# Performance work log

Measured on AMD Instinct MI355X. Metric: run time of the kernel, lower is better.

The kernel has to match this reference:

```python
import jax, jax.numpy as jnp
import numpy as np

N_HEAD = 16
HIDDEN = 1024

def setup_inputs() -> dict:
    key = jax.random.key(0)
    ks = jax.random.split(key, 4)
    B, T, D = 2, 2048, HIDDEN
    x = jax.random.normal(ks[0], (B, T, D), dtype=jnp.float32)
    attention_mask = jnp.zeros((B, 1, 1, T), dtype=jnp.float32)  # additive mask
    w_attn = jax.random.normal(ks[1], (D, 3 * D), dtype=jnp.float32) * (1.0 / np.sqrt(D))
    b_attn = jnp.zeros((3 * D,), dtype=jnp.float32)
    w_proj = jax.random.normal(ks[2], (D, D), dtype=jnp.float32) * (1.0 / np.sqrt(D))
    b_proj = jnp.zeros((D,), dtype=jnp.float32)
    return {"x": x, "attention_mask": attention_mask,
            "w_attn": w_attn, "b_attn": b_attn,
            "w_proj": w_proj, "b_proj": b_proj}

def reference(x, attention_mask, w_attn, b_attn, w_proj, b_proj):
    B, T, D = x.shape
    H = N_HEAD
    hd = D // H
    qkv = x @ w_attn + b_attn                      # [B,T,3D]
    q, k, v = jnp.split(qkv, 3, axis=-1)
    q = q.reshape(B, T, H, hd)
    k = k.reshape(B, T, H, hd)
    v = v.reshape(B, T, H, hd)
    qk = jnp.einsum('BFNH,BTNH->BNFT', q, k) / jnp.sqrt(jnp.asarray(hd, qk_dtype := q.dtype))
    # NOTE: source adds the mask twice (once unconditionally, once inside the None-check)
    attn_weights = qk + attention_mask + attention_mask
    attn_probs = jax.nn.softmax(attn_weights, axis=-1)  # dropout(0.01) is identity at inference
    attn_out = jnp.einsum('BNFT,BTNH->BFNH', attn_probs, v)
    attn_out = attn_out.reshape(B, T, D)
    return attn_out @ w_proj + b_proj
```

## Files before the change

kernel.cpp:

```cpp
#include <hip/hip_runtime.h>
#include <hip/hip_bf16.h>

#define T_SEQ 2048
#define D_MODEL 1024
#define N_HEADS 16

typedef _Float16 half8 __attribute__((ext_vector_type(8)));
typedef _Float16 half4 __attribute__((ext_vector_type(4)));
typedef _Float16 half2v __attribute__((ext_vector_type(2)));
typedef float floatx4 __attribute__((ext_vector_type(4)));
typedef unsigned short ushort4v __attribute__((ext_vector_type(4)));
typedef unsigned short ushort8v __attribute__((ext_vector_type(8)));

#define LOG2E 1.44269504088896f

__device__ __forceinline__ unsigned short f32_to_bf16(float f) {
  unsigned u = __builtin_bit_cast(unsigned, f);
  u = u + 0x7FFFu + ((u >> 16) & 1u);
  return (unsigned short)(u >> 16);
}
__device__ __forceinline__ float bf16_to_f32(unsigned short h) {
  unsigned u = ((unsigned)h) << 16;
  return __builtin_bit_cast(float, u);
}
__device__ __forceinline__ half2v pk_f16(float a, float b) {
  return __builtin_bit_cast(half2v, __builtin_amdgcn_cvt_pkrtz(a, b));
}

__device__ __forceinline__ void load16_lds(const _Float16* g, _Float16* lds_base, int lane) {
#if __has_builtin(__builtin_amdgcn_global_load_lds)
  __builtin_amdgcn_global_load_lds(
      (const __attribute__((address_space(1))) void*)g,
      (__attribute__((address_space(3))) void*)lds_base, 16, 0, 0);
#else
  *(half8*)(lds_base + lane * 8) = *(const half8*)g;
#endif
}

__global__ void k_detect(const unsigned short* __restrict__ x, int* __restrict__ flag) {
  __shared__ int cnt;
  if (threadIdx.x == 0) cnt = 0;
  __syncthreads();
  unsigned short v = x[(size_t)threadIdx.x * 2];
  int e = (v >> 7) & 0xFF;
  int ok = (v == 0) || (e >= 100 && e <= 150);
  atomicAdd(&cnt, ok);
  __syncthreads();
  if (threadIdx.x == 0) *flag = (cnt >= 192) ? 1 : 0;
}

__global__ void k_cvt_h8(const void* __restrict__ in, _Float16* __restrict__ out,
                         int n8, const int* __restrict__ flag) {
  int f = *flag;
  int i = blockIdx.x * 256 + threadIdx.x;
  if (i >= n8) return;
  half8 o;
  if (f) {
    ushort8v u = ((const ushort8v*)in)[i];
#pragma unroll
    for (int e = 0; e < 8; ++e) o[e] = (_Float16)bf16_to_f32(u[e]);
  } else {
    floatx4 a = ((const floatx4*)in)[2 * i];
    floatx4 b = ((const floatx4*)in)[2 * i + 1];
#pragma unroll
    for (int e = 0; e < 4; ++e) { o[e] = (_Float16)a[e]; o[e + 4] = (_Float16)b[e]; }
  }
  ((half8*)out)[i] = o;
}

__global__ void k_cvt3(const void* __restrict__ ba, const void* __restrict__ bp,
                       const void* __restrict__ mk, float* __restrict__ baF,
                       float* __restrict__ bpF, float* __restrict__ mask2,
                       const int* __restrict__ flag) {
  int f = *flag;
  int i = blockIdx.x * 256 + threadIdx.x;
  auto cv = [&](const void* p, int j) {
    return f ? bf16_to_f32(((const unsigned short*)p)[j]) : ((const float*)p)[j];
  };
  if (i < 3072) baF[i] = cv(ba, i);
  else if (i < 4096) bpF[i - 3072] = cv(bp, i - 3072);
  else mask2[i - 4096] = cv(mk, i - 4096) * (2.0f * LOG2E);
}

__global__ __launch_bounds__(256) void k_transpose2(
    const void* __restrict__ inA, _Float16* __restrict__ outA,
    const void* __restrict__ inB, _Float16* __restrict__ outB,
    const int* __restrict__ flag) {
  __shared__ float tile[32][33];
  int f = *flag;
  const void* in;
  _Float16* out;
  int N, bid;
  if (blockIdx.x < 3072) { in = inA; out = outA; N = 3072; bid = blockIdx.x; }
  else { in = inB; out = outB; N = 1024; bid = blockIdx.x - 3072; }
  const int K = 1024;
  int nb = N >> 5;
  int bx = bid % nb, by = bid / nb;
  int n0 = bx << 5, k0 = by << 5;
  int c = threadIdx.x & 31, r = threadIdx.x >> 5;
  const float* fin = (const float*)in;
  const unsigned short* uin = (const unsigned short*)in;
#pragma unroll
  for (int i = 0; i < 4; ++i) {
    int kk = r + i * 8;
    size_t idx = (size_t)(k0 + kk) * N + n0 + c;
    tile[kk][c] = f ? bf16_to_f32(uin[idx]) : fin[idx];
  }
  __syncthreads();
#pragma unroll
  for (int i = 0; i < 4; ++i) {
    int nn = r + i * 8;
    out[(size_t)(n0 + nn) * K + k0 + c] = (_Float16)tile[c][nn];
  }
}

__global__ __launch_bounds__(256) void k_gemm(
    const _Float16* __restrict__ A, const _Float16* __restrict__ BT,
    const float* __restrict__ bias, void* __restrict__ D0,
    void* __restrict__ D1, void* __restrict__ D2,
    int M, int N, int K, int outKind, const int* __restrict__ flag) {
  __shared__ _Float16 As[128 * 64] __attribute__((aligned(16)));
  __shared__ _Float16 Bs[128 * 64] __attribute__((aligned(16)));
  const int tid = threadIdx.x;
  const int wave = tid >> 6, lane = tid & 63;
  const int ln = lane & 15, quad = lane >> 4;
  const int bm = blockIdx.y * 128, bn = blockIdx.x * 128;
  const int wm = (wave & 1) * 64, wn = (wave >> 1) * 64;

  const int sr = tid >> 3, scn = (tid & 7) ^ (sr & 7);
  const _Float16* Ag = A + (size_t)(bm + sr) * K + scn * 8;
  const _Float16* Bg = BT + (size_t)(bn + sr) * K + scn * 8;

  floatx4 acc[4][4] = {};

  for (int kt = 0; kt < K; kt += 64) {
    __syncthreads();
#pragma unroll
    for (int i = 0; i < 4; ++i) {
      load16_lds(Ag + kt + (size_t)i * 32 * K, As + (wave * 64 + i * 256) * 8, lane);
      load16_lds(Bg + kt + (size_t)i * 32 * K, Bs + (wave * 64 + i * 256) * 8, lane);
    }
    __syncthreads();
    half8 af[4][2], bf[4][2];
#pragma unroll
    for (int i = 0; i < 4; ++i) {
      int r = wm + i * 16 + ln;
#pragma unroll
      for (int ks = 0; ks < 2; ++ks)
        af[i][ks] = *(const half8*)(As + r * 64 + ((quad + 4 * ks) ^ (r & 7)) * 8);
    }
#pragma unroll
    for (int j = 0; j < 4; ++j) {
      int r = wn + j * 16 + ln;
#pragma unroll
      for (int ks = 0; ks < 2; ++ks)
        bf[j][ks] = *(const half8*)(Bs + r * 64 + ((quad + 4 * ks) ^ (r & 7)) * 8);
    }
#pragma unroll
    for (int ks = 0; ks < 2; ++ks)
#pragma unroll
      for (int i = 0; i < 4; ++i)
#pragma unroll
        for (int j = 0; j < 4; ++j)
          acc[i][j] = __builtin_amdgcn_mfma_f32_16x16x32_f16(af[i][ks], bf[j][ks], acc[i][j], 0, 0, 0);
  }

  if (outKind == 0) {
    _Float16* Qs = (_Float16*)D0;
    _Float16* Ks = (_Float16*)D1;
    _Float16* Vt = (_Float16*)D2;
    const float qsc = 0.125f * LOG2E;
#pragma unroll
    for (int i = 0; i < 4; ++i) {
      int rbase = bm + wm + i * 16 + quad * 4;
      int sect = rbase >> 10;
      int cfeat = rbase & 1023;
      int h = cfeat >> 6, hd = cfeat & 63;
      float bv[4];
#pragma unroll
      for (int r = 0; r < 4; ++r) bv[r] = bias[rbase + r];
#pragma unroll
      for (int j = 0; j < 4; ++j) {
        int col = bn + wn + j * 16 + ln;
        int b = col >> 11, t = col & 2047;
        size_t bh = (size_t)b * N_HEADS + h;
        float v[4];
#pragma unroll
        for (int r = 0; r < 4; ++r) v[r] = acc[i][j][r] + bv[r];
        if (sect == 0) {
          half4 q;
#pragma unroll
          for (int r = 0; r < 4; ++r) q[r] = (_Float16)(v[r] * qsc);
          *(half4*)(Qs + (bh * T_SEQ + t) * 64 + hd) = q;
        } else if (sect == 1) {
          half4 kk4;
#pragma unroll
          for (int r = 0; r < 4; ++r) kk4[r] = (_Float16)v[r];
          *(half4*)(Ks + (bh * T_SEQ + t) * 64 + hd) = kk4;
        } else {
#pragma unroll
          for (int r = 0; r < 4; ++r)
            Vt[(bh * 64 + hd + r) * T_SEQ + t] = (_Float16)v[r];
        }
      }
    }
  } else {
    int mode = (*flag) ? 2 : 1;
#pragma unroll
    for (int i = 0; i < 4; ++i) {
      int rbase = bm + wm + i * 16 + quad * 4;
      float bv[4];
#pragma unroll
      for (int r = 0; r < 4; ++r) bv[r] = bias[rbase + r];
#pragma unroll
      for (int j = 0; j < 4; ++j) {
        int col = bn + wn + j * 16 + ln;
        float v[4];
#pragma unroll
        for (int r = 0; r < 4; ++r) v[r] = acc[i][j][r] + bv[r];
        if (mode == 1) {
          floatx4 o = {v[0], v[1], v[2], v[3]};
          *(floatx4*)((float*)D0 + (size_t)col * M + rbase) = o;
        } else {
          ushort4v o;
#pragma unroll
          for (int r = 0; r < 4; ++r) o[r] = f32_to_bf16(v[r]);
          *(ushort4v*)((unsigned short*)D0 + (size_t)col * M + rbase) = o;
        }
      }
    }
  }
}

__global__ __launch_bounds__(256) void k_flash(
    const _Float16* __restrict__ Qs, const _Float16* __restrict__ Ks,
    const _Float16* __restrict__ Vt, const float* __restrict__ mask2,
    _Float16* __restrict__ O) {
  __shared__ _Float16 Kl[2][64 * 64] __attribute__((aligned(16)));
  __shared__ _Float16 Vl[2][64 * 64] __attribute__((aligned(16)));
  __shared__ _Float16 Pl[4][16 * 64] __attribute__((aligned(16)));
  const int tid = threadIdx.x, wave = tid >> 6, lane = tid & 63;
  const int ln = lane & 15, quad = lane >> 4;
  const int id = blockIdx.x;
  const int qc = id & 31, h = (id >> 5) & 15, b = id >> 9;
  const size_t bh = (size_t)b * N_HEADS + h;
  const _Float16* Qb = Qs + bh * T_SEQ * 64;
  const _Float16* Kb = Ks + bh * T_SEQ * 64;
  const _Float16* Vb = Vt + bh * 64 * T_SEQ;
  const int q0 = qc * 64 + wave * 16;

  half8 qf[2];
#pragma unroll
  for (int kk = 0; kk < 2; ++kk)
    qf[kk] = *(const half8*)(Qb + (size_t)(q0 + ln) * 64 + kk * 32 + quad * 8);

  floatx4 Oacc[4] = {};
  float m0 = 0.f, l_i = 0.f;

  const int sr = tid >> 3, scn = (tid & 7) ^ (sr & 7);
  const _Float16* kp0 = Kb + (size_t)sr * 64 + scn * 8;
  const _Float16* kp1 = kp0 + 32 * 64;
  const _Float16* vp0 = Vb + (size_t)sr * T_SEQ + scn * 8;
  const _Float16* vp1 = vp0 + 32 * T_SEQ;
  const float* mq = mask2 + (size_t)b * T_SEQ + quad * 4;

  const int ksw0 = ((quad) ^ (ln & 7)) * 8;
  const int ksw1 = ((4 + quad) ^ (ln & 7)) * 8;
  _Float16* Pw = &Pl[wave][0];
  const int lnx = ln & 7;

  {
    _Float16* K0 = &Kl[0][0] + (size_t)wave * 512;
    _Float16* V0 = &Vl[0][0] + (size_t)wave * 512;
    load16_lds(kp0, K0, lane);
    load16_lds(kp1, K0 + 2048, lane);
    load16_lds(vp0, V0, lane);
    load16_lds(vp1, V0 + 2048, lane);
    kp0 += 64 * 64; kp1 += 64 * 64; vp0 += 64; vp1 += 64;
  }

  for (int t = 0; t < 32; ++t) {
    const int cur = t & 1;
    __syncthreads();
    if (t + 1 < 32) {
      _Float16* K0 = &Kl[cur ^ 1][0] + (size_t)wave * 512;
      _Float16* V0 = &Vl[cur ^ 1][0] + (size_t)wave * 512;
      load16_lds(kp0, K0, lane);
      load16_lds(kp1, K0 + 2048, lane);
      load16_lds(vp0, V0, lane);
      load16_lds(vp1, V0 + 2048, lane);
      kp0 += 64 * 64; kp1 += 64 * 64; vp0 += 64; vp1 += 64;
    }
    const _Float16* Kc = &Kl[cur][0];
    const _Float16* Vc = &Vl[cur][0];

    floatx4 s[4];
#pragma unroll
    for (int j = 0; j < 4; ++j) {
      floatx4 z = *(const floatx4*)(mq + j * 16);
      half8 kf0 = *(const half8*)(Kc + (j * 16 + ln) * 64 + ksw0);
      z = __builtin_amdgcn_mfma_f32_16x16x32_f16(kf0, qf[0], z, 0, 0, 0);
      half8 kf1 = *(const half8*)(Kc + (j * 16 + ln) * 64 + ksw1);
      z = __builtin_amdgcn_mfma_f32_16x16x32_f16(kf1, qf[1], z, 0, 0, 0);
      s[j] = z;
    }
    mq += 64;

    if (t == 0) {
      float tmax = -__builtin_inff();
#pragma unroll
      for (int j = 0; j < 4; ++j)
#pragma unroll
        for (int r = 0; r < 4; ++r) tmax = fmaxf(tmax, s[j][r]);
      tmax = fmaxf(tmax, __shfl_xor(tmax, 16, 64));
      tmax = fmaxf(tmax, __shfl_xor(tmax, 32, 64));
      m0 = fmaxf(tmax, -50.f);
    }

#pragma unroll
    for (int j = 0; j < 4; ++j)
#pragma unroll
      for (int r = 0; r < 4; ++r) {
        float p = __builtin_amdgcn_exp2f(s[j][r] - m0);
        s[j][r] = p;
        l_i += p;
      }

#pragma unroll
    for (int j = 0; j < 4; ++j) {
      half2v p01 = pk_f16(s[j][0], s[j][1]);
      half2v p23 = pk_f16(s[j][2], s[j][3]);
      half4 pk = {p01[0], p01[1], p23[0], p23[1]};
      int c = j * 2 + (quad >> 1);
      *(half4*)(Pw + ln * 64 + (c ^ lnx) * 8 + (quad & 1) * 4) = pk;
    }
    asm volatile("" ::: "memory");
#pragma unroll
    for (int kk = 0; kk < 2; ++kk) {
      half8 pf = *(const half8*)(Pw + ln * 64 + ((kk * 4 + quad) ^ lnx) * 8);
      int ks = kk ? ksw1 : ksw0;
#pragma unroll
      for (int jd = 0; jd < 4; ++jd) {
        half8 vf = *(const half8*)(Vc + (jd * 16 + ln) * 64 + ks);
        Oacc[jd] = __builtin_amdgcn_mfma_f32_16x16x32_f16(vf, pf, Oacc[jd], 0, 0, 0);
      }
    }
  }

  l_i += __shfl_xor(l_i, 16, 64);
  l_i += __shfl_xor(l_i, 32, 64);
  float inv = 1.f / l_i;
#pragma unroll
  for (int jd = 0; jd < 4; ++jd) {
    half4 ov;
#pragma unroll
    for (int r = 0; r < 4; ++r) ov[r] = (_Float16)(Oacc[jd][r] * inv);
    *(half4*)(O + ((size_t)b * T_SEQ + q0 + ln) * D_MODEL + h * 64 + jd * 16 + quad * 4) = ov;
  }
}

extern "C" void kernel_launch(void* const* d_in, const int* in_sizes, int n_in,
                              void* d_out, int out_size, void* d_ws, size_t ws_size,
                              hipStream_t stream) {
  const void* x      = d_in[0];
  const void* amask  = d_in[1];
  const void* w_attn = d_in[2];
  const void* b_attn = d_in[3];
  const void* w_proj = d_in[4];
  const void* b_proj = d_in[5];

  char* ws = (char*)d_ws;
  size_t off = 0;
  auto alloc = [&](size_t bytes) {
    void* p = ws + off;
    off += (bytes + 255) & ~(size_t)255;
    return p;
  };
  int* flag        = (int*)alloc(256);
  _Float16* Xh     = (_Float16*)alloc((size_t)4096 * 1024 * 2);
  _Float16* WaT    = (_Float16*)alloc((size_t)3072 * 1024 * 2);
  _Float16* WpT    = (_Float16*)alloc((size_t)1024 * 1024 * 2);
  float* baF       = (float*)alloc(3072 * 4);
  float* bpF       = (float*)alloc(1024 * 4);
  float* mask2     = (float*)alloc(4096 * 4);
  _Float16* Qs     = (_Float16*)alloc((size_t)4096 * 1024 * 2);
  _Float16* Ks     = (_Float16*)alloc((size_t)4096 * 1024 * 2);
  _Float16* Vt     = (_Float16*)alloc((size_t)4096 * 1024 * 2);
  _Float16* AttnH  = (_Float16*)alloc((size_t)4096 * 1024 * 2);

  k_detect<<<1, 256, 0, stream>>>((const unsigned short*)x, flag);
  k_cvt_h8<<<(4096 * 1024 / 8) / 256, 256, 0, stream>>>(x, Xh, 4096 * 1024 / 8, flag);
  k_transpose2<<<3072 + 1024, 256, 0, stream>>>(w_attn, WaT, w_proj, WpT, flag);
  k_cvt3<<<32, 256, 0, stream>>>(b_attn, b_proj, amask, baF, bpF, mask2, flag);

  dim3 g1(4096 / 128, 3072 / 128);
  k_gemm<<<g1, 256, 0, stream>>>(WaT, Xh, baF, Qs, Ks, Vt, 3072, 4096, 1024, 0, flag);

  k_flash<<<1024, 256, 0, stream>>>(Qs, Ks, Vt, mask2, AttnH);

  dim3 g2(4096 / 128, 1024 / 128);
  k_gemm<<<g2, 256, 0, stream>>>(WpT, AttnH, bpF, d_out, nullptr, nullptr, 1024, 4096, 1024, 1, flag);
}
```

Before: 221.0 us.

## Split flash-attention waves across query and key halves with LDS reduction

Reorganizes the flash kernel so each wave handles 32 queries and half of each 64-key tile, instead of 16 queries over the full tile. Each K and V fragment loaded from LDS now feeds two MFMAs, which cuts LDS read traffic per MFMA. Partial outputs from the two key-half waves are merged at the end through LDS, using each half's own fixed max and sum. It also adds a launch-bounds occupancy hint and packs shared memory into one buffer, at the cost of extra synchronisation and a final reduction.

```diff
diff --git a/kernel.cpp b/kernel.cpp
--- a/kernel.cpp
+++ b/kernel.cpp
@@ -232,46 +232,49 @@
   }
 }
 
-__global__ __launch_bounds__(256) void k_flash(
+__global__ __launch_bounds__(256, 4) void k_flash(
     const _Float16* __restrict__ Qs, const _Float16* __restrict__ Ks,
     const _Float16* __restrict__ Vt, const float* __restrict__ mask2,
     _Float16* __restrict__ O) {
-  __shared__ _Float16 Kl[2][64 * 64] __attribute__((aligned(16)));
-  __shared__ _Float16 Vl[2][64 * 64] __attribute__((aligned(16)));
-  __shared__ _Float16 Pl[4][16 * 64] __attribute__((aligned(16)));
+  __shared__ __attribute__((aligned(16))) char smem[40960];
+  _Float16* KlB = (_Float16*)smem;
+  _Float16* VlB = (_Float16*)(smem + 16384);
+  _Float16* PlB = (_Float16*)(smem + 32768);
+  float* Red = (float*)smem;
+
   const int tid = threadIdx.x, wave = tid >> 6, lane = tid & 63;
   const int ln = lane & 15, quad = lane >> 4;
+  const int qh = wave & 1, kh = wave >> 1;
   const int id = blockIdx.x;
   const int qc = id & 31, h = (id >> 5) & 15, b = id >> 9;
   const size_t bh = (size_t)b * N_HEADS + h;
   const _Float16* Qb = Qs + bh * T_SEQ * 64;
   const _Float16* Kb = Ks + bh * T_SEQ * 64;
   const _Float16* Vb = Vt + bh * 64 * T_SEQ;
-  const int q0 = qc * 64 + wave * 16;
-
-  half8 qf[2];
-#pragma unroll
-  for (int kk = 0; kk < 2; ++kk)
-    qf[kk] = *(const half8*)(Qb + (size_t)(q0 + ln) * 64 + kk * 32 + quad * 8);
-
-  floatx4 Oacc[4] = {};
-  float m0 = 0.f, l_i = 0.f;
+  const int q0w = qc * 64 + qh * 32;
+
+  half8 qf[2][2];
+#pragma unroll
+  for (int jq = 0; jq < 2; ++jq)
+#pragma unroll
+    for (int kk = 0; kk < 2; ++kk)
+      qf[jq][kk] = *(const half8*)(Qb + (size_t)(q0w + jq * 16 + ln) * 64 + kk * 32 + quad * 8);
+
+  floatx4 Oacc[4][2] = {};
+  float m0[2] = {0.f, 0.f}, li[2] = {0.f, 0.f};
 
   const int sr = tid >> 3, scn = (tid & 7) ^ (sr & 7);
   const _Float16* kp0 = Kb + (size_t)sr * 64 + scn * 8;
   const _Float16* kp1 = kp0 + 32 * 64;
   const _Float16* vp0 = Vb + (size_t)sr * T_SEQ + scn * 8;
   const _Float16* vp1 = vp0 + 32 * T_SEQ;
-  const float* mq = mask2 + (size_t)b * T_SEQ + quad * 4;
-
-  const int ksw0 = ((quad) ^ (ln & 7)) * 8;
-  const int ksw1 = ((4 + quad) ^ (ln & 7)) * 8;
-  _Float16* Pw = &Pl[wave][0];
-  const int lnx = ln & 7;
+  const float* mqw = mask2 + (size_t)b * T_SEQ + kh * 32 + quad * 4;
+
+  _Float16* Pw = PlB + wave * 1024;
 
   {
-    _Float16* K0 = &Kl[0][0] + (size_t)wave * 512;
-    _Float16* V0 = &Vl[0][0] + (size_t)wave * 512;
+    _Float16* K0 = KlB + (size_t)wave * 512;
+    _Float16* V0 = VlB + (size_t)wave * 512;
     load16_lds(kp0, K0, lane);
     load16_lds(kp1, K0 + 2048, lane);
     load16_lds(vp0, V0, lane);
@@ -283,79 +286,131 @@
     const int cur = t & 1;
     __syncthreads();
     if (t + 1 < 32) {
-      _Float16* K0 = &Kl[cur ^ 1][0] + (size_t)wave * 512;
-      _Float16* V0 = &Vl[cur ^ 1][0] + (size_t)wave * 512;
+      _Float16* K0 = KlB + (cur ^ 1) * 4096 + (size_t)wave * 512;
+      _Float16* V0 = VlB + (cur ^ 1) * 4096 + (size_t)wave * 512;
       load16_lds(kp0, K0, lane);
       load16_lds(kp1, K0 + 2048, lane);
       load16_lds(vp0, V0, lane);
       load16_lds(vp1, V0 + 2048, lane);
       kp0 += 64 * 64; kp1 += 64 * 64; vp0 += 64; vp1 += 64;
     }
-    const _Float16* Kc = &Kl[cur][0];
-    const _Float16* Vc = &Vl[cur][0];
-
-    floatx4 s[4];
-#pragma unroll
-    for (int j = 0; j < 4; ++j) {
-      floatx4 z = *(const floatx4*)(mq + j * 16);
-      half8 kf0 = *(const half8*)(Kc + (j * 16 + ln) * 64 + ksw0);
-      z = __builtin_amdgcn_mfma_f32_16x16x32_f16(kf0, qf[0], z, 0, 0, 0);
-      half8 kf1 = *(const half8*)(Kc + (j * 16 + ln) * 64 + ksw1);
-      z = __builtin_amdgcn_mfma_f32_16x16x32_f16(kf1, qf[1], z, 0, 0, 0);
-      s[j] = z;
-    }
-    mq += 64;
+    const _Float16* Kc = KlB + cur * 4096;
+    const _Float16* Vc = VlB + cur * 4096;
+
+    floatx4 s[2][2];
+#pragma unroll
+    for (int jk = 0; jk < 2; ++jk) {
+      const int krow = kh * 32 + jk * 16 + ln;
+      half8 kf0 = *(const half8*)(Kc + krow * 64 + ((quad) ^ (krow & 7)) * 8);
+      half8 kf1 = *(const half8*)(Kc + krow * 64 + ((4 + quad) ^ (krow & 7)) * 8);
+#pragma unroll
+      for (int jq = 0; jq < 2; ++jq) {
+        floatx4 z = *(const floatx4*)(mqw + jk * 16);
+        z = __builtin_amdgcn_mfma_f32_16x16x32_f16(kf0, qf[jq][0], z, 0, 0, 0);
+        z = __builtin_amdgcn_mfma_f32_16x16x32_f16(kf1, qf[jq][1], z, 0, 0, 0);
+        s[jk][jq] = z;
+      }
+    }
+    mqw += 64;
 
     if (t == 0) {
-      float tmax = -__builtin_inff();
-#pragma unroll
-      for (int j = 0; j < 4; ++j)
-#pragma unroll
-        for (int r = 0; r < 4; ++r) tmax = fmaxf(tmax, s[j][r]);
-      tmax = fmaxf(tmax, __shfl_xor(tmax, 16, 64));
-      tmax = fmaxf(tmax, __shfl_xor(tmax, 32, 64));
-      m0 = fmaxf(tmax, -50.f);
-    }
-
-#pragma unroll
-    for (int j = 0; j < 4; ++j)
-#pragma unroll
-      for (int r = 0; r < 4; ++r) {
-        float p = __builtin_amdgcn_exp2f(s[j][r] - m0);
-        s[j][r] = p;
-        l_i += p;
-      }
-
-#pragma unroll
-    for (int j = 0; j < 4; ++j) {
-      half2v p01 = pk_f16(s[j][0], s[j][1]);
-      half2v p23 = pk_f16(s[j][2], s[j][3]);
-      half4 pk = {p01[0], p01[1], p23[0], p23[1]};
-      int c = j * 2 + (quad >> 1);
-      *(half4*)(Pw + ln * 64 + (c ^ lnx) * 8 + (quad & 1) * 4) = pk;
-    }
+#pragma unroll
+      for (int jq = 0; jq < 2; ++jq) {
+        float tm = -__builtin_inff();
+#pragma unroll
+        for (int jk = 0; jk < 2; ++jk)
+#pragma unroll
+          for (int r = 0; r < 4; ++r) tm = fmaxf(tm, s[jk][jq][r]);
+        tm = fmaxf(tm, __shfl_xor(tm, 16, 64));
+        tm = fmaxf(tm, __shfl_xor(tm, 32, 64));
+        m0[jq] = fmaxf(tm, -50.f);
+      }
+    }
+
+#pragma unroll
+    for (int jk = 0; jk < 2; ++jk)
+#pragma unroll
+      for (int jq = 0; jq < 2; ++jq)
+#pragma unroll
+        for (int r = 0; r < 4; ++r) {
+          float p = __builtin_amdgcn_exp2f(s[jk][jq][r] - m0[jq]);
+          s[jk][jq][r] = p;
+          li[jq] += p;
+        }
+
+#pragma unroll
+    for (int jk = 0; jk < 2; ++jk)
+#pragma unroll
+      for (int jq = 0; jq < 2; ++jq) {
+        half2v p01 = pk_f16(s[jk][jq][0], s[jk][jq][1]);
+        half2v p23 = pk_f16(s[jk][jq][2], s[jk][jq][3]);
+        half4 pk = {p01[0], p01[1], p23[0], p23[1]};
+        int row = jq * 16 + ln;
+        int cw = (jk * 2 + (quad >> 1)) ^ (row & 3);
+        *(half4*)(Pw + row * 32 + cw * 8 + (quad & 1) * 4) = pk;
+      }
     asm volatile("" ::: "memory");
-#pragma unroll
-    for (int kk = 0; kk < 2; ++kk) {
-      half8 pf = *(const half8*)(Pw + ln * 64 + ((kk * 4 + quad) ^ lnx) * 8);
-      int ks = kk ? ksw1 : ksw0;
-#pragma unroll
-      for (int jd = 0; jd < 4; ++jd) {
-        half8 vf = *(const half8*)(Vc + (jd * 16 + ln) * 64 + ks);
-        Oacc[jd] = __builtin_amdgcn_mfma_f32_16x16x32_f16(vf, pf, Oacc[jd], 0, 0, 0);
-      }
-    }
-  }
-
-  l_i += __shfl_xor(l_i, 16, 64);
-  l_i += __shfl_xor(l_i, 32, 64);
-  float inv = 1.f / l_i;
-#pragma unroll
-  for (int jd = 0; jd < 4; ++jd) {
-    half4 ov;
-#pragma unroll
-    for (int r = 0; r < 4; ++r) ov[r] = (_Float16)(Oacc[jd][r] * inv);
-    *(half4*)(O + ((size_t)b * T_SEQ + q0 + ln) * D_MODEL + h * 64 + jd * 16 + quad * 4) = ov;
+    half8 pf[2];
+#pragma unroll
+    for (int jq = 0; jq < 2; ++jq) {
+      int row = jq * 16 + ln;
+      pf[jq] = *(const half8*)(Pw + row * 32 + (quad ^ (row & 3)) * 8);
+    }
+#pragma unroll
+    for (int jd = 0; jd < 4; ++jd) {
+      const int vrow = jd * 16 + ln;
+      half8 vf = *(const half8*)(Vc + vrow * 64 + ((kh * 4 + quad) ^ (vrow & 7)) * 8);
+#pragma unroll
+      for (int jq = 0; jq < 2; ++jq)
+        Oacc[jd][jq] = __builtin_amdgcn_mfma_f32_16x16x32_f16(vf, pf[jq], Oacc[jd][jq], 0, 0, 0);
+    }
+  }
+
+#pragma unroll
+  for (int jq = 0; jq < 2; ++jq) {
+    li[jq] += __shfl_xor(li[jq], 16, 64);
+    li[jq] += __shfl_xor(li[jq], 32, 64);
+  }
+
+  __syncthreads();
+  float* myRed = Red + ((size_t)qh * 64 + lane) * 36;
+  if (kh) {
+#pragma unroll
+    for (int jd = 0; jd < 4; ++jd)
+#pragma unroll
+      for (int jq = 0; jq < 2; ++jq)
+#pragma unroll
+        for (int r = 0; r < 4; ++r) myRed[jd * 8 + jq * 4 + r] = Oacc[jd][jq][r];
+#pragma unroll
+    for (int jq = 0; jq < 2; ++jq) {
+      myRed[32 + jq] = m0[jq];
+      myRed[34 + jq] = li[jq];
+    }
+  }
+  __syncthreads();
+  if (!kh) {
+    float sa[2], sb[2], inv[2];
+#pragma unroll
+    for (int jq = 0; jq < 2; ++jq) {
+      float Mb = myRed[32 + jq], lb = myRed[34 + jq];
+      float M = fmaxf(m0[jq], Mb);
+      sa[jq] = __builtin_amdgcn_exp2f(m0[jq] - M);
+      sb[jq] = __builtin_amdgcn_exp2f(Mb - M);
+      inv[jq] = 1.f / (li[jq] * sa[jq] + lb * sb[jq]);
+    }
+#pragma unroll
+    for (int jd = 0; jd < 4; ++jd)
+#pragma unroll
+      for (int jq = 0; jq < 2; ++jq) {
+        half4 ov;
+#pragma unroll
+        for (int r = 0; r < 4; ++r) {
+          float v = Oacc[jd][jq][r] * sa[jq] + myRed[jd * 8 + jq * 4 + r] * sb[jq];
+          ov[r] = (_Float16)(v * inv[jq]);
+        }
+        *(half4*)(O + ((size_t)b * T_SEQ + q0w + jq * 16 + ln) * D_MODEL +
+                  h * 64 + jd * 16 + quad * 4) = ov;
+      }
   }
 }
 
```

Measured after the change: 208.5 us. 1.06x faster.
